# Kernel tuning notes

Hardware: AMD Instinct MI355X
Metric: run time of the kernel (lower is better)

Reference implementation:

```python
import jax, jax.numpy as jnp
import numpy as np

N = 100000          # number of graph nodes
NNZ = 1_600_000     # edges (nnz of sparse adjacency), avg degree 16
D_IN = 512
D_OUT = 128


def setup_inputs() -> dict:
    key = jax.random.key(0)
    kx, kw, kv, kr, kc = jax.random.split(key, 5)
    stdv = 1.0 / np.sqrt(D_IN)  # matches module's init(): uniform(-stdv, stdv)
    x = jax.random.normal(kx, (N, D_IN), dtype=jnp.float32)
    W = jax.random.uniform(kw, (D_IN, D_OUT), minval=-stdv, maxval=stdv, dtype=jnp.float32)
    b = jnp.zeros((D_OUT,), dtype=jnp.float32)
    # Sparse adjacency in COO form: adj[row[e], col[e]] = vals[e]
    vals = jax.random.uniform(kv, (NNZ,), dtype=jnp.float32)
    row = jax.random.randint(kr, (NNZ,), 0, N, dtype=jnp.int64)
    col = jax.random.randint(kc, (NNZ,), 0, N, dtype=jnp.int64)
    return {"x": x, "W": W, "b": b, "vals": vals, "row": row, "col": col}


def reference(x, W, b, vals, row, col):
    # support = self.W(input)  -> dense linear projection [N, D_OUT]
    support = x @ W + b
    # output = torch.spmm(adj, support): out[r] = sum_e adj[r, c_e] * support[c_e]
    msgs = vals[:, None] * support[col]          # [NNZ, D_OUT] gather + scale
    out = jax.ops.segment_sum(msgs, row, num_segments=x.shape[0])  # scatter-add
    return out
```

## Files before the change

kernel.cpp:

```cpp
#include <hip/hip_runtime.h>
#include <hip/hip_bf16.h>

#define D_IN  512
#define D_OUT 128
#define FB_SHIFT 7
#define SB_SHIFT 14
#define NB_S 8
#define MAXFB 800
#define NFH 800
#define CHUNK 4096
#define CAP2 2560
#define MAXE (CAP2 / 256)

typedef __attribute__((ext_vector_type(8))) short bf16x8;
typedef __attribute__((ext_vector_type(4))) float f32x4;
typedef __attribute__((ext_vector_type(8))) short s16x8;

static __device__ inline short f2bs(float f) {
    __hip_bfloat16 h = __float2bfloat16(f);
    return *reinterpret_cast<short*>(&h);
}

__global__ __launch_bounds__(256) void wt_prep(const float* __restrict__ W,
                                               short* __restrict__ Wt,
                                               int* __restrict__ fhist) {
    int idx = blockIdx.x * 256 + threadIdx.x;
    if (idx < D_IN * D_OUT) {
        int k = idx >> 7, c = idx & 127;
        Wt[(long)c * D_IN + k] = f2bs(W[idx]);
    }
    if (blockIdx.x == 0)
        for (int i = threadIdx.x; i < NFH; i += 256) fhist[i] = 0;
}

__global__ __launch_bounds__(256) void fhist_kernel(const int* __restrict__ row,
                                                    int* __restrict__ fhist,
                                                    int nnz, int nfb) {
    __shared__ int lh[NFH];
    const int t = threadIdx.x;
    for (int i = t; i < nfb; i += 256) lh[i] = 0;
    __syncthreads();
    const int base = blockIdx.x * CHUNK;
    const int end = min(base + CHUNK, nnz);
    for (int i = base + t; i < end; i += 256)
        atomicAdd(&lh[row[i] >> FB_SHIFT], 1);
    __syncthreads();
    for (int i = t; i < nfb; i += 256) {
        int c = lh[i];
        if (c) atomicAdd(&fhist[i], c);
    }
}

__global__ __launch_bounds__(256) void fscan(const int* __restrict__ fhist,
                                             int* __restrict__ foffs,
                                             int* __restrict__ scursor,
                                             int* __restrict__ gcursor,
                                             int nfb, int nnz) {
    __shared__ int sdata[256];
    const int t = threadIdx.x;
    int c[4]; int s = 0;
#pragma unroll
    for (int j = 0; j < 4; ++j) {
        int i = t * 4 + j;
        c[j] = (i < nfb) ? fhist[i] : 0;
        s += c[j];
    }
    sdata[t] = s;
    __syncthreads();
    for (int off = 1; off < 256; off <<= 1) {
        int v = (t >= off) ? sdata[t - off] : 0;
        __syncthreads();
        sdata[t] += v;
        __syncthreads();
    }
    int excl = (t == 0) ? 0 : sdata[t - 1];
#pragma unroll
    for (int j = 0; j < 4; ++j) {
        int i = t * 4 + j;
        if (i < nfb) {
            foffs[i] = excl;
            gcursor[i] = excl;
            if ((i & 127) == 0) scursor[i >> 7] = excl;
        }
        excl += c[j];
    }
    if (t == 0) foffs[nfb] = nnz;
}

__global__ __launch_bounds__(256) void sscatter(
    const int* __restrict__ row, const int* __restrict__ col,
    const float* __restrict__ vals, int* __restrict__ scursor,
    int2* __restrict__ evt, int nnz)
{
    __shared__ int hist[NB_S], lbase[NB_S], gbase[NB_S], lcur[NB_S];
    __shared__ int2 stage[CHUNK];
    const int t = threadIdx.x;
    const int base = blockIdx.x * CHUNK;
    const int nloc = min(CHUNK, nnz - base);
    if (t < NB_S) hist[t] = 0;
    __syncthreads();

    int myr[CHUNK / 256];
#pragma unroll
    for (int j = 0; j < CHUNK / 256; ++j) {
        int e = base + t + j * 256;
        myr[j] = (e < nnz) ? row[e] : -1;
        if (myr[j] >= 0) atomicAdd(&hist[myr[j] >> SB_SHIFT], 1);
    }
    __syncthreads();
    if (t == 0) {
        int run = 0;
#pragma unroll
        for (int s = 0; s < NB_S; ++s) {
            lbase[s] = run; lcur[s] = run;
            int c = hist[s];
            gbase[s] = c ? atomicAdd(&scursor[s], c) : 0;
            run += c;
        }
    }
    __syncthreads();
#pragma unroll
    for (int j = 0; j < CHUNK / 256; ++j) {
        int e = base + t + j * 256;
        if (e < nnz) {
            int slot = atomicAdd(&lcur[myr[j] >> SB_SHIFT], 1);
            stage[slot] = make_int2(((myr[j] & 16383) << 17) | col[e],
                                    __float_as_int(vals[e]));
        }
    }
    __syncthreads();
#pragma unroll
    for (int j = 0; j < CHUNK / 256; ++j) {
        int s = t + j * 256;
        if (s < nloc) {
            int sb = 0;
#pragma unroll
            for (int q = 1; q < NB_S; ++q) if (s >= lbase[q]) sb = q;
            evt[gbase[sb] + (s - lbase[sb])] = stage[s];
        }
    }
}

__global__ __launch_bounds__(256) void fscatter(
    const int2* __restrict__ evt, const int* __restrict__ foffs,
    int* __restrict__ gcursor, int2* __restrict__ ev, int nnz, int nfb)
{
    __shared__ int hist[MAXFB], lbase[MAXFB], gbase[MAXFB];
    __shared__ int ssum[256];
    __shared__ int sbpos[NB_S + 1];
    __shared__ int2 stage[CHUNK];
    __shared__ short sbkt[CHUNK];
    const int t = threadIdx.x;
    const int base = blockIdx.x * CHUNK;
    const int nloc = min(CHUNK, nnz - base);

    for (int i = t; i < nfb; i += 256) hist[i] = 0;
    if (t <= NB_S) {
        int fi = t << 7;
        sbpos[t] = foffs[fi > nfb ? nfb : fi];
    }
    __syncthreads();

    int2 mypay[CHUNK / 256];
    int myfb[CHUNK / 256];
#pragma unroll
    for (int j = 0; j < CHUNK / 256; ++j) {
        int p = base + t + j * 256;
        if (p < nnz) {
            mypay[j] = evt[p];
            int sb = 0;
#pragma unroll
            for (int q = 1; q < NB_S; ++q) if (p >= sbpos[q]) sb = q;
            myfb[j] = sb * 128 + ((mypay[j].x >> 17) >> 7);
            atomicAdd(&hist[myfb[j]], 1);
        } else myfb[j] = -1;
    }
    __syncthreads();

    int c[4], s = 0;
#pragma unroll
    for (int j = 0; j < 4; ++j) {
        int i = t * 4 + j;
        c[j] = (i < nfb) ? hist[i] : 0;
        s += c[j];
    }
    ssum[t] = s;
    __syncthreads();
    for (int off = 1; off < 256; off <<= 1) {
        int v = (t >= off) ? ssum[t - off] : 0;
        __syncthreads();
        ssum[t] += v;
        __syncthreads();
    }
    int excl = (t == 0) ? 0 : ssum[t - 1];
#pragma unroll
    for (int j = 0; j < 4; ++j) {
        int i = t * 4 + j;
        if (i < nfb) {
            lbase[i] = excl;
            gbase[i] = c[j] ? atomicAdd(&gcursor[i], c[j]) : 0;
        }
        excl += c[j];
    }
    __syncthreads();
    for (int i = t; i < nfb; i += 256) hist[i] = lbase[i];
    __syncthreads();

#pragma unroll
    for (int j = 0; j < CHUNK / 256; ++j) {
        if (myfb[j] >= 0) {
            int slot = atomicAdd(&hist[myfb[j]], 1);
            stage[slot] = mypay[j];
            sbkt[slot] = (short)myfb[j];
        }
    }
    __syncthreads();
#pragma unroll
    for (int j = 0; j < CHUNK / 256; ++j) {
        int s2 = t + j * 256;
        if (s2 < nloc) {
            int fb = sbkt[s2];
            ev[gbase[fb] + (s2 - lbase[fb])] = stage[s2];
        }
    }
}

__global__ __launch_bounds__(256) void bspmm(
    const int* __restrict__ foffs, const int2* __restrict__ ev,
    const __hip_bfloat16* __restrict__ supb, float* __restrict__ out, int n)
{
    __shared__ int rcnt[128];
    __shared__ int rbase[129];
    __shared__ int lcur[128];
    __shared__ int2 stage[CAP2];
    const int bk = blockIdx.x;
    const int t = threadIdx.x;
    const int r0 = bk << FB_SHIFT;
    const int rend = min(r0 + 128, n);
    const int nrow = rend - r0;
    const int g0 = foffs[bk];
    const int g1 = foffs[bk + 1];
    const int ne = g1 - g0;

    const int w   = t >> 6, l = t & 63;
    const int g   = l >> 4;
    const int sub = l & 15;

    if (ne <= CAP2) {
        if (t < 128) rcnt[t] = 0;
        __syncthreads();
        int2 myq[MAXE]; int myrl[MAXE];
#pragma unroll
        for (int j = 0; j < MAXE; ++j) {
            int i = t + j * 256;
            myrl[j] = -1;
            if (i < ne) {
                myq[j] = ev[g0 + i];
                myrl[j] = (myq[j].x >> 17) & 127;
                atomicAdd(&rcnt[myrl[j]], 1);
            }
        }
        __syncthreads();
        if (t < 128) lcur[t] = rcnt[t];
        __syncthreads();
        for (int off = 1; off < 128; off <<= 1) {
            int u = (t < 128 && t >= off) ? lcur[t - off] : 0;
            __syncthreads();
            if (t < 128) lcur[t] += u;
            __syncthreads();
        }
        if (t < 128) rbase[t + 1] = lcur[t];
        if (t == 0) rbase[0] = 0;
        __syncthreads();
        if (t < 128) lcur[t] = rbase[t];
        __syncthreads();
#pragma unroll
        for (int j = 0; j < MAXE; ++j) {
            if (myrl[j] >= 0) {
                int slot = atomicAdd(&lcur[myrl[j]], 1);
                stage[slot] = myq[j];
            }
        }
        __syncthreads();

        for (int rr = w; rr < nrow; rr += 4) {
            const int r = r0 + rr;
            const int e0 = rbase[rr];
            const int e1 = rbase[rr + 1];
            float acc[8];
#pragma unroll
            for (int i = 0; i < 8; ++i) acc[i] = 0.f;

            auto fma_edge = [&](const int2 q) {
                const s16x8 sv = *reinterpret_cast<const s16x8*>(
                    supb + (long)(q.x & 0x1FFFF) * D_OUT + sub * 8);
                const float v = __int_as_float(q.y);
                const __hip_bfloat162* hp = reinterpret_cast<const __hip_bfloat162*>(&sv);
#pragma unroll
                for (int i = 0; i < 4; ++i) {
                    const float2 f = __bfloat1622float2(hp[i]);
                    acc[2 * i]     += v * f.x;
                    acc[2 * i + 1] += v * f.y;
                }
            };

            int e = e0;
            for (; e + 16 <= e1; e += 16) {
                const int2 q0 = stage[e + g];
                const int2 q1 = stage[e + 4 + g];
                const int2 q2 = stage[e + 8 + g];
                const int2 q3 = stage[e + 12 + g];
                fma_edge(q0); fma_edge(q1); fma_edge(q2); fma_edge(q3);
            }
            for (; e + 4 <= e1; e += 4) {
                fma_edge(stage[e + g]);
            }
            const int rem = e1 - e;
            if (g < rem) fma_edge(stage[e + g]);

#pragma unroll
            for (int i = 0; i < 8; ++i) {
                acc[i] += __shfl_xor(acc[i], 16);
                acc[i] += __shfl_xor(acc[i], 32);
            }
            if (g == 0) {
                float4 o0 = make_float4(acc[0], acc[1], acc[2], acc[3]);
                float4 o1 = make_float4(acc[4], acc[5], acc[6], acc[7]);
                float* op = out + (long)r * D_OUT + sub * 8;
                *reinterpret_cast<float4*>(op) = o0;
                *reinterpret_cast<float4*>(op + 4) = o1;
            }
        }
    } else {
        for (int rr = w; rr < nrow; rr += 4) {
            const int r = r0 + rr;
            const int rl = r & 127;
            float ax = 0.f, ay = 0.f;
            for (int e = g0; e < g1; ++e) {
                const int2 q = ev[e];
                if (((q.x >> 17) & 127) == rl) {
                    const float v = __int_as_float(q.y);
                    const __hip_bfloat162 sh = *reinterpret_cast<const __hip_bfloat162*>(
                        supb + (long)(q.x & 0x1FFFF) * D_OUT + l * 2);
                    const float2 f = __bfloat1622float2(sh);
                    ax += v * f.x;
                    ay += v * f.y;
                }
            }
            *reinterpret_cast<float2*>(out + (long)r * D_OUT + l * 2) =
                make_float2(ax, ay);
        }
    }
}

__global__ __launch_bounds__(256) void gemm_mfma(
    const float* __restrict__ x,
    const short* __restrict__ Wt,
    const float* __restrict__ b,
    __hip_bfloat16* __restrict__ supb,
    int n_nodes)
{
    __shared__ s16x8 A_c[2][4 * 128];
    __shared__ s16x8 B_c[2][4 * 128];

    const int tid  = threadIdx.x;
    const int wave = tid >> 6;
    const int lane = tid & 63;
    const int ln16 = lane & 15;
    const int kb   = lane >> 4;
    const int row0 = blockIdx.x * 128;

    const int srow = tid >> 2;
    const int skc  = tid & 3;

    float4 areg[2][2];
    s16x8  breg[2];

    auto load_A = [&](int k0) {
#pragma unroll
        for (int j = 0; j < 2; ++j) {
            int r = row0 + srow + j * 64;
            r = (r < n_nodes) ? r : (n_nodes - 1);
            const float* p = x + (long)r * D_IN + k0 + skc * 8;
            areg[j][0] = *reinterpret_cast<const float4*>(p);
            areg[j][1] = *reinterpret_cast<const float4*>(p + 4);
        }
    };
    auto load_B = [&](int k0) {
#pragma unroll
        for (int j = 0; j < 2; ++j) {
            int c = srow + j * 64;
            breg[j] = *reinterpret_cast<const s16x8*>(Wt + (long)c * D_IN + k0 + skc * 8);
        }
    };
    auto write_AB = [&](int buf) {
#pragma unroll
        for (int j = 0; j < 2; ++j) {
            const int r = srow + j * 64;
            s16x8 v;
            v[0] = f2bs(areg[j][0].x); v[1] = f2bs(areg[j][0].y);
            v[2] = f2bs(areg[j][0].z); v[3] = f2bs(areg[j][0].w);
            v[4] = f2bs(areg[j][1].x); v[5] = f2bs(areg[j][1].y);
            v[6] = f2bs(areg[j][1].z); v[7] = f2bs(areg[j][1].w);
            A_c[buf][skc * 128 + (r ^ skc)] = v;
            B_c[buf][skc * 128 + (r ^ skc)] = breg[j];
        }
    };

    f32x4 acc[2][8];
#pragma unroll
    for (int rg = 0; rg < 2; ++rg)
#pragma unroll
        for (int t = 0; t < 8; ++t) acc[rg][t] = (f32x4){0.f, 0.f, 0.f, 0.f};

    auto compute = [&](int buf) {
        bf16x8 af[2];
#pragma unroll
        for (int rg = 0; rg < 2; ++rg) {
            const int r = wave * 32 + rg * 16 + ln16;
            const s16x8 v = A_c[buf][kb * 128 + (r ^ kb)];
            af[rg] = *reinterpret_cast<const bf16x8*>(&v);
        }
#pragma unroll
        for (int t = 0; t < 8; ++t) {
            const int c = t * 16 + ln16;
            const s16x8 vb = B_c[buf][kb * 128 + (c ^ kb)];
            const bf16x8 bf = *reinterpret_cast<const bf16x8*>(&vb);
            acc[0][t] = __builtin_amdgcn_mfma_f32_16x16x32_bf16(af[0], bf, acc[0][t], 0, 0, 0);
            acc[1][t] = __builtin_amdgcn_mfma_f32_16x16x32_bf16(af[1], bf, acc[1][t], 0, 0, 0);
        }
    };

    load_A(0);
    load_B(0);
    write_AB(0);
    __syncthreads();

    for (int ks = 0; ks < 15; ++ks) {
        const int cur = ks & 1, nxt = cur ^ 1;
        load_A((ks + 1) * 32);
        load_B((ks + 1) * 32);
        compute(cur);
        write_AB(nxt);
        __syncthreads();
    }
    compute(1);

#pragma unroll
    for (int t = 0; t < 8; ++t) {
        const int col = t * 16 + ln16;
        const float bias = b[col];
#pragma unroll
        for (int rg = 0; rg < 2; ++rg) {
#pragma unroll
            for (int r = 0; r < 4; ++r) {
                const int rr = row0 + wave * 32 + rg * 16 + kb * 4 + r;
                if (rr < n_nodes)
                    supb[(long)rr * D_OUT + col] = __float2bfloat16(acc[rg][t][r] + bias);
            }
        }
    }
}

__global__ __launch_bounds__(256) void spmm_atomic(
    const __hip_bfloat16* __restrict__ supb, const float* __restrict__ vals,
    const int* __restrict__ row, const int* __restrict__ col,
    float* __restrict__ out, int nnz)
{
    long gidx = (long)blockIdx.x * 256 + threadIdx.x;
    int e = (int)(gidx >> 7);
    int d = (int)(gidx & 127);
    if (e < nnz) {
        atomicAdd(&out[(long)row[e] * D_OUT + d],
                  vals[e] * __bfloat162float(supb[(long)col[e] * D_OUT + d]));
    }
}

extern "C" void kernel_launch(void* const* d_in, const int* in_sizes, int n_in,
                              void* d_out, int out_size, void* d_ws, size_t ws_size,
                              hipStream_t stream) {
    const float* x    = (const float*)d_in[0];
    const float* W    = (const float*)d_in[1];
    const float* b    = (const float*)d_in[2];
    const float* vals = (const float*)d_in[3];
    const int*   row  = (const int*)d_in[4];
    const int*   col  = (const int*)d_in[5];
    float* out = (float*)d_out;

    const int n_nodes = in_sizes[0] / D_IN;
    const int nnz     = in_sizes[3];
    const int nfb     = (n_nodes + 127) >> FB_SHIFT;

    auto align_up = [](size_t v) { return (v + 255) & ~(size_t)255; };
    char* wsb = (char*)d_ws;
    size_t off = 0;
    __hip_bfloat16* supb = (__hip_bfloat16*)(wsb + off);
    off = align_up(off + (size_t)n_nodes * D_OUT * 2);
    short* Wt = (short*)(wsb + off);
    off = align_up(off + (size_t)D_OUT * D_IN * 2);
    const size_t need_fallback = off;
    int* fhist   = (int*)(wsb + off); off = align_up(off + (size_t)NFH * 4);
    int* foffs   = (int*)(wsb + off); off = align_up(off + (size_t)(nfb + 1) * 4);
    int* scursor = (int*)(wsb + off); off = align_up(off + NB_S * 4);
    int* gcursor = (int*)(wsb + off); off = align_up(off + (size_t)nfb * 4);
    int2* evt    = (int2*)(wsb + off); off = align_up(off + (size_t)nnz * 8);
    int2* ev     = (int2*)(wsb + off); off = align_up(off + (size_t)nnz * 8);
    const size_t need_full = off;

    if (ws_size >= need_full && nfb <= MAXFB) {
        const int nchunks = (nnz + CHUNK - 1) / CHUNK;
        wt_prep<<<dim3((D_IN * D_OUT) / 256), dim3(256), 0, stream>>>(W, Wt, fhist);
        fhist_kernel<<<dim3(nchunks), dim3(256), 0, stream>>>(row, fhist, nnz, nfb);
        fscan<<<dim3(1), dim3(256), 0, stream>>>(fhist, foffs, scursor, gcursor,
                                                 nfb, nnz);
        gemm_mfma<<<dim3((n_nodes + 127) / 128), dim3(256), 0, stream>>>(
            x, Wt, b, supb, n_nodes);
        sscatter<<<dim3(nchunks), dim3(256), 0, stream>>>(
            row, col, vals, scursor, evt, nnz);
        fscatter<<<dim3(nchunks), dim3(256), 0, stream>>>(
            evt, foffs, gcursor, ev, nnz, nfb);
        bspmm<<<dim3(nfb), dim3(256), 0, stream>>>(foffs, ev, supb, out, n_nodes);
    } else if (ws_size >= need_fallback) {
        wt_prep<<<dim3((D_IN * D_OUT) / 256), dim3(256), 0, stream>>>(W, Wt, fhist);
        gemm_mfma<<<dim3((n_nodes + 127) / 128), dim3(256), 0, stream>>>(
            x, Wt, b, supb, n_nodes);
        hipMemsetAsync(out, 0, (size_t)out_size * 4, stream);
        long total = (long)nnz * D_OUT;
        spmm_atomic<<<dim3((int)((total + 255) / 256)), dim3(256), 0, stream>>>(
            supb, vals, row, col, out, nnz);
    }
}
```

Measured before the change: 222.8 us.

## Fuse edge histogram, scan and two scatter passes into one cooperative kernel

```diff
diff --git a/kernel.cpp b/kernel.cpp
--- a/kernel.cpp
+++ b/kernel.cpp
@@ -1,5 +1,8 @@
 #include <hip/hip_runtime.h>
 #include <hip/hip_bf16.h>
+#include <hip/hip_cooperative_groups.h>
+
+namespace cg = cooperative_groups;
 
 #define D_IN  512
 #define D_OUT 128
@@ -7,7 +10,6 @@
 #define SB_SHIFT 14
 #define NB_S 8
 #define MAXFB 800
-#define NFH 800
 #define CHUNK 4096
 #define CAP2 2560
 #define MAXE (CAP2 / 256)
@@ -22,99 +24,99 @@
 }
 
 __global__ __launch_bounds__(256) void wt_prep(const float* __restrict__ W,
-                                               short* __restrict__ Wt,
-                                               int* __restrict__ fhist) {
+                                               short* __restrict__ Wt) {
     int idx = blockIdx.x * 256 + threadIdx.x;
-    if (idx < D_IN * D_OUT) {
-        int k = idx >> 7, c = idx & 127;
-        Wt[(long)c * D_IN + k] = f2bs(W[idx]);
-    }
-    if (blockIdx.x == 0)
-        for (int i = threadIdx.x; i < NFH; i += 256) fhist[i] = 0;
-}
-
-__global__ __launch_bounds__(256) void fhist_kernel(const int* __restrict__ row,
-                                                    int* __restrict__ fhist,
-                                                    int nnz, int nfb) {
-    __shared__ int lh[NFH];
+    int k = idx >> 7, c = idx & 127;
+    Wt[(long)c * D_IN + k] = f2bs(W[idx]);
+}
+
+__global__ __launch_bounds__(256, 2) void edge_pipe(
+    const int* __restrict__ row, const int* __restrict__ col,
+    const float* __restrict__ vals,
+    int* __restrict__ fhist, int* __restrict__ foffs,
+    int* __restrict__ scursor, int* __restrict__ gcursor,
+    int2* __restrict__ evt, int2* __restrict__ ev,
+    int nnz, int nfb)
+{
+    __shared__ int2 stage[CHUNK];
+    __shared__ short sbkt[CHUNK];
+    __shared__ int hA[MAXFB];
+    __shared__ int hB[MAXFB];
+    __shared__ int hC[MAXFB];
+    __shared__ int ssum[256];
+    __shared__ int sbpos[NB_S + 1];
+    __shared__ int sh[NB_S], slb[NB_S], sgb[NB_S], slc[NB_S];
+
     const int t = threadIdx.x;
-    for (int i = t; i < nfb; i += 256) lh[i] = 0;
-    __syncthreads();
-    const int base = blockIdx.x * CHUNK;
-    const int end = min(base + CHUNK, nnz);
-    for (int i = base + t; i < end; i += 256)
-        atomicAdd(&lh[row[i] >> FB_SHIFT], 1);
-    __syncthreads();
-    for (int i = t; i < nfb; i += 256) {
-        int c = lh[i];
-        if (c) atomicAdd(&fhist[i], c);
-    }
-}
-
-__global__ __launch_bounds__(256) void fscan(const int* __restrict__ fhist,
-                                             int* __restrict__ foffs,
-                                             int* __restrict__ scursor,
-                                             int* __restrict__ gcursor,
-                                             int nfb, int nnz) {
-    __shared__ int sdata[256];
-    const int t = threadIdx.x;
-    int c[4]; int s = 0;
-#pragma unroll
-    for (int j = 0; j < 4; ++j) {
-        int i = t * 4 + j;
-        c[j] = (i < nfb) ? fhist[i] : 0;
-        s += c[j];
-    }
-    sdata[t] = s;
-    __syncthreads();
-    for (int off = 1; off < 256; off <<= 1) {
-        int v = (t >= off) ? sdata[t - off] : 0;
-        __syncthreads();
-        sdata[t] += v;
-        __syncthreads();
-    }
-    int excl = (t == 0) ? 0 : sdata[t - 1];
-#pragma unroll
-    for (int j = 0; j < 4; ++j) {
-        int i = t * 4 + j;
-        if (i < nfb) {
-            foffs[i] = excl;
-            gcursor[i] = excl;
-            if ((i & 127) == 0) scursor[i >> 7] = excl;
-        }
-        excl += c[j];
-    }
-    if (t == 0) foffs[nfb] = nnz;
-}
-
-__global__ __launch_bounds__(256) void sscatter(
-    const int* __restrict__ row, const int* __restrict__ col,
-    const float* __restrict__ vals, int* __restrict__ scursor,
-    int2* __restrict__ evt, int nnz)
-{
-    __shared__ int hist[NB_S], lbase[NB_S], gbase[NB_S], lcur[NB_S];
-    __shared__ int2 stage[CHUNK];
-    const int t = threadIdx.x;
-    const int base = blockIdx.x * CHUNK;
+    const int blk = blockIdx.x;
+    const int base = blk * CHUNK;
     const int nloc = min(CHUNK, nnz - base);
-    if (t < NB_S) hist[t] = 0;
-    __syncthreads();
-
+    cg::grid_group grid = cg::this_grid();
+
+    for (int i = t; i < nfb; i += 256) hA[i] = 0;
+    __syncthreads();
     int myr[CHUNK / 256];
 #pragma unroll
     for (int j = 0; j < CHUNK / 256; ++j) {
         int e = base + t + j * 256;
         myr[j] = (e < nnz) ? row[e] : -1;
-        if (myr[j] >= 0) atomicAdd(&hist[myr[j] >> SB_SHIFT], 1);
-    }
+        if (myr[j] >= 0) atomicAdd(&hA[myr[j] >> FB_SHIFT], 1);
+    }
+    if (blk == 0)
+        for (int i = t; i < nfb; i += 256) fhist[i] = 0;
+    __syncthreads();
+    grid.sync();
+
+    for (int i = t; i < nfb; i += 256) {
+        int c = hA[i];
+        if (c) atomicAdd(&fhist[i], c);
+    }
+    grid.sync();
+
+    if (blk == 0) {
+        int c[4]; int s = 0;
+#pragma unroll
+        for (int j = 0; j < 4; ++j) {
+            int i = t * 4 + j;
+            c[j] = (i < nfb) ? fhist[i] : 0;
+            s += c[j];
+        }
+        ssum[t] = s;
+        __syncthreads();
+        for (int off = 1; off < 256; off <<= 1) {
+            int v = (t >= off) ? ssum[t - off] : 0;
+            __syncthreads();
+            ssum[t] += v;
+            __syncthreads();
+        }
+        int excl = (t == 0) ? 0 : ssum[t - 1];
+#pragma unroll
+        for (int j = 0; j < 4; ++j) {
+            int i = t * 4 + j;
+            if (i < nfb) {
+                foffs[i] = excl;
+                gcursor[i] = excl;
+                if ((i & 127) == 0) scursor[i >> 7] = excl;
+            }
+            excl += c[j];
+        }
+        if (t == 0) foffs[nfb] = nnz;
+    }
+    grid.sync();
+
+    if (t < NB_S) sh[t] = 0;
+    __syncthreads();
+#pragma unroll
+    for (int j = 0; j < CHUNK / 256; ++j)
+        if (myr[j] >= 0) atomicAdd(&sh[myr[j] >> SB_SHIFT], 1);
     __syncthreads();
     if (t == 0) {
         int run = 0;
 #pragma unroll
-        for (int s = 0; s < NB_S; ++s) {
-            lbase[s] = run; lcur[s] = run;
-            int c = hist[s];
-            gbase[s] = c ? atomicAdd(&scursor[s], c) : 0;
+        for (int s2 = 0; s2 < NB_S; ++s2) {
+            slb[s2] = run; slc[s2] = run;
+            int c = sh[s2];
+            sgb[s2] = c ? atomicAdd(&scursor[s2], c) : 0;
             run += c;
         }
     }
@@ -122,8 +124,8 @@
 #pragma unroll
     for (int j = 0; j < CHUNK / 256; ++j) {
         int e = base + t + j * 256;
-        if (e < nnz) {
-            int slot = atomicAdd(&lcur[myr[j] >> SB_SHIFT], 1);
+        if (myr[j] >= 0) {
+            int slot = atomicAdd(&slc[myr[j] >> SB_SHIFT], 1);
             stage[slot] = make_int2(((myr[j] & 16383) << 17) | col[e],
                                     __float_as_int(vals[e]));
         }
@@ -131,36 +133,22 @@
     __syncthreads();
 #pragma unroll
     for (int j = 0; j < CHUNK / 256; ++j) {
-        int s = t + j * 256;
-        if (s < nloc) {
+        int s2 = t + j * 256;
+        if (s2 < nloc) {
             int sb = 0;
 #pragma unroll
-            for (int q = 1; q < NB_S; ++q) if (s >= lbase[q]) sb = q;
-            evt[gbase[sb] + (s - lbase[sb])] = stage[s];
-        }
-    }
-}
-
-__global__ __launch_bounds__(256) void fscatter(
-    const int2* __restrict__ evt, const int* __restrict__ foffs,
-    int* __restrict__ gcursor, int2* __restrict__ ev, int nnz, int nfb)
-{
-    __shared__ int hist[MAXFB], lbase[MAXFB], gbase[MAXFB];
-    __shared__ int ssum[256];
-    __shared__ int sbpos[NB_S + 1];
-    __shared__ int2 stage[CHUNK];
-    __shared__ short sbkt[CHUNK];
-    const int t = threadIdx.x;
-    const int base = blockIdx.x * CHUNK;
-    const int nloc = min(CHUNK, nnz - base);
-
-    for (int i = t; i < nfb; i += 256) hist[i] = 0;
+            for (int q = 1; q < NB_S; ++q) if (s2 >= slb[q]) sb = q;
+            evt[sgb[sb] + (s2 - slb[sb])] = stage[s2];
+        }
+    }
+    grid.sync();
+
+    for (int i = t; i < nfb; i += 256) hA[i] = 0;
     if (t <= NB_S) {
         int fi = t << 7;
         sbpos[t] = foffs[fi > nfb ? nfb : fi];
     }
     __syncthreads();
-
     int2 mypay[CHUNK / 256];
     int myfb[CHUNK / 256];
 #pragma unroll
@@ -172,19 +160,18 @@
 #pragma unroll
             for (int q = 1; q < NB_S; ++q) if (p >= sbpos[q]) sb = q;
             myfb[j] = sb * 128 + ((mypay[j].x >> 17) >> 7);
-            atomicAdd(&hist[myfb[j]], 1);
+            atomicAdd(&hA[myfb[j]], 1);
         } else myfb[j] = -1;
     }
     __syncthreads();
-
-    int c[4], s = 0;
+    int c2[4], s3 = 0;
 #pragma unroll
     for (int j = 0; j < 4; ++j) {
         int i = t * 4 + j;
-        c[j] = (i < nfb) ? hist[i] : 0;
-        s += c[j];
-    }
-    ssum[t] = s;
+        c2[j] = (i < nfb) ? hA[i] : 0;
+        s3 += c2[j];
+    }
+    ssum[t] = s3;
     __syncthreads();
     for (int off = 1; off < 256; off <<= 1) {
         int v = (t >= off) ? ssum[t - off] : 0;
@@ -192,24 +179,23 @@
         ssum[t] += v;
         __syncthreads();
     }
-    int excl = (t == 0) ? 0 : ssum[t - 1];
+    int excl2 = (t == 0) ? 0 : ssum[t - 1];
 #pragma unroll
     for (int j = 0; j < 4; ++j) {
         int i = t * 4 + j;
         if (i < nfb) {
-            lbase[i] = excl;
-            gbase[i] = c[j] ? atomicAdd(&gcursor[i], c[j]) : 0;
-        }
-        excl += c[j];
-    }
-    __syncthreads();
-    for (int i = t; i < nfb; i += 256) hist[i] = lbase[i];
-    __syncthreads();
-
+            hB[i] = excl2;
+            hC[i] = c2[j] ? atomicAdd(&gcursor[i], c2[j]) : 0;
+        }
+        excl2 += c2[j];
+    }
+    __syncthreads();
+    for (int i = t; i < nfb; i += 256) hA[i] = hB[i];
+    __syncthreads();
 #pragma unroll
     for (int j = 0; j < CHUNK / 256; ++j) {
         if (myfb[j] >= 0) {
-            int slot = atomicAdd(&hist[myfb[j]], 1);
+            int slot = atomicAdd(&hA[myfb[j]], 1);
             stage[slot] = mypay[j];
             sbkt[slot] = (short)myfb[j];
         }
@@ -220,7 +206,7 @@
         int s2 = t + j * 256;
         if (s2 < nloc) {
             int fb = sbkt[s2];
-            ev[gbase[fb] + (s2 - lbase[fb])] = stage[s2];
+            ev[hC[fb] + (s2 - hB[fb])] = stage[s2];
         }
     }
 }
@@ -340,9 +326,9 @@
                 const int2 q = ev[e];
                 if (((q.x >> 17) & 127) == rl) {
                     const float v = __int_as_float(q.y);
-                    const __hip_bfloat162 sh = *reinterpret_cast<const __hip_bfloat162*>(
+                    const __hip_bfloat162 sh2 = *reinterpret_cast<const __hip_bfloat162*>(
                         supb + (long)(q.x & 0x1FFFF) * D_OUT + l * 2);
-                    const float2 f = __bfloat1622float2(sh);
+                    const float2 f = __bfloat1622float2(sh2);
                     ax += v * f.x;
                     ay += v * f.y;
                 }
@@ -488,8 +474,8 @@
     float* out = (float*)d_out;
 
     const int n_nodes = in_sizes[0] / D_IN;
-    const int nnz     = in_sizes[3];
-    const int nfb     = (n_nodes + 127) >> FB_SHIFT;
+    int nnz           = in_sizes[3];
+    int nfb           = (n_nodes + 127) >> FB_SHIFT;
 
     auto align_up = [](size_t v) { return (v + 255) & ~(size_t)255; };
     char* wsb = (char*)d_ws;
@@ -499,7 +485,7 @@
     short* Wt = (short*)(wsb + off);
     off = align_up(off + (size_t)D_OUT * D_IN * 2);
     const size_t need_fallback = off;
-    int* fhist   = (int*)(wsb + off); off = align_up(off + (size_t)NFH * 4);
+    int* fhist   = (int*)(wsb + off); off = align_up(off + (size_t)MAXFB * 4);
     int* foffs   = (int*)(wsb + off); off = align_up(off + (size_t)(nfb + 1) * 4);
     int* scursor = (int*)(wsb + off); off = align_up(off + NB_S * 4);
     int* gcursor = (int*)(wsb + off); off = align_up(off + (size_t)nfb * 4);
@@ -509,19 +495,18 @@
 
     if (ws_size >= need_full && nfb <= MAXFB) {
         const int nchunks = (nnz + CHUNK - 1) / CHUNK;
-        wt_prep<<<dim3((D_IN * D_OUT) / 256), dim3(256), 0, stream>>>(W, Wt, fhist);
-        fhist_kernel<<<dim3(nchunks), dim3(256), 0, stream>>>(row, fhist, nnz, nfb);
-        fscan<<<dim3(1), dim3(256), 0, stream>>>(fhist, foffs, scursor, gcursor,
-                                                 nfb, nnz);
+        wt_prep<<<dim3((D_IN * D_OUT) / 256), dim3(256), 0, stream>>>(W, Wt);
         gemm_mfma<<<dim3((n_nodes + 127) / 128), dim3(256), 0, stream>>>(
             x, Wt, b, supb, n_nodes);
-        sscatter<<<dim3(nchunks), dim3(256), 0, stream>>>(
-            row, col, vals, scursor, evt, nnz);
-        fscatter<<<dim3(nchunks), dim3(256), 0, stream>>>(
-            evt, foffs, gcursor, ev, nnz, nfb);
+        void* args[] = {(void*)&row, (void*)&col, (void*)&vals,
+                        (void*)&fhist, (void*)&foffs, (void*)&scursor,
+                        (void*)&gcursor, (void*)&evt, (void*)&ev,
+                        (void*)&nnz, (void*)&nfb};
+        hipLaunchCooperativeKernel((void*)edge_pipe, dim3(nchunks), dim3(256),
+                                   args, 0, stream);
         bspmm<<<dim3(nfb), dim3(256), 0, stream>>>(foffs, ev, supb, out, n_nodes);
     } else if (ws_size >= need_fallback) {
-        wt_prep<<<dim3((D_IN * D_OUT) / 256), dim3(256), 0, stream>>>(W, Wt, fhist);
+        wt_prep<<<dim3((D_IN * D_OUT) / 256), dim3(256), 0, stream>>>(W, Wt);
         gemm_mfma<<<dim3((n_nodes + 127) / 128), dim3(256), 0, stream>>>(
             x, Wt, b, supb, n_nodes);
         hipMemsetAsync(out, 0, (size_t)out_size * 4, stream);
```

Measured after the change: 387.2 us. 1.74x slower.

## Merge weight prep with histogram and fold scan into GEMM launch

Applied to the files above, without the earlier changes.

```diff
diff --git a/kernel.cpp b/kernel.cpp
--- a/kernel.cpp
+++ b/kernel.cpp
@@ -21,70 +21,190 @@
     return *reinterpret_cast<short*>(&h);
 }
 
-__global__ __launch_bounds__(256) void wt_prep(const float* __restrict__ W,
-                                               short* __restrict__ Wt,
-                                               int* __restrict__ fhist) {
-    int idx = blockIdx.x * 256 + threadIdx.x;
-    if (idx < D_IN * D_OUT) {
+__global__ __launch_bounds__(256) void prep_hist(
+    const float* __restrict__ W, short* __restrict__ Wt,
+    const int* __restrict__ row, int* __restrict__ bhist,
+    int nnz, int nfb, int nwt)
+{
+    __shared__ int lh[NFH];
+    const int t = threadIdx.x;
+    if ((int)blockIdx.x < nwt) {
+        int idx = blockIdx.x * 256 + t;
         int k = idx >> 7, c = idx & 127;
         Wt[(long)c * D_IN + k] = f2bs(W[idx]);
-    }
-    if (blockIdx.x == 0)
-        for (int i = threadIdx.x; i < NFH; i += 256) fhist[i] = 0;
-}
-
-__global__ __launch_bounds__(256) void fhist_kernel(const int* __restrict__ row,
-                                                    int* __restrict__ fhist,
-                                                    int nnz, int nfb) {
-    __shared__ int lh[NFH];
-    const int t = threadIdx.x;
+        return;
+    }
+    const int cb = blockIdx.x - nwt;
     for (int i = t; i < nfb; i += 256) lh[i] = 0;
     __syncthreads();
-    const int base = blockIdx.x * CHUNK;
+    const int base = cb * CHUNK;
     const int end = min(base + CHUNK, nnz);
     for (int i = base + t; i < end; i += 256)
         atomicAdd(&lh[row[i] >> FB_SHIFT], 1);
     __syncthreads();
-    for (int i = t; i < nfb; i += 256) {
-        int c = lh[i];
-        if (c) atomicAdd(&fhist[i], c);
-    }
-}
-
-__global__ __launch_bounds__(256) void fscan(const int* __restrict__ fhist,
-                                             int* __restrict__ foffs,
-                                             int* __restrict__ scursor,
-                                             int* __restrict__ gcursor,
-                                             int nfb, int nnz) {
-    __shared__ int sdata[256];
-    const int t = threadIdx.x;
-    int c[4]; int s = 0;
-#pragma unroll
-    for (int j = 0; j < 4; ++j) {
-        int i = t * 4 + j;
-        c[j] = (i < nfb) ? fhist[i] : 0;
-        s += c[j];
-    }
-    sdata[t] = s;
-    __syncthreads();
-    for (int off = 1; off < 256; off <<= 1) {
-        int v = (t >= off) ? sdata[t - off] : 0;
-        __syncthreads();
-        sdata[t] += v;
-        __syncthreads();
-    }
-    int excl = (t == 0) ? 0 : sdata[t - 1];
-#pragma unroll
-    for (int j = 0; j < 4; ++j) {
-        int i = t * 4 + j;
-        if (i < nfb) {
-            foffs[i] = excl;
-            gcursor[i] = excl;
-            if ((i & 127) == 0) scursor[i >> 7] = excl;
-        }
-        excl += c[j];
-    }
-    if (t == 0) foffs[nfb] = nnz;
+    for (int i = t; i < nfb; i += 256)
+        bhist[(size_t)cb * NFH + i] = lh[i];
+}
+
+__global__ __launch_bounds__(256) void gemm_fscan(
+    const float* __restrict__ x,
+    const short* __restrict__ Wt,
+    const float* __restrict__ b,
+    __hip_bfloat16* __restrict__ supb,
+    int n_nodes,
+    const int* __restrict__ bhist,
+    int* __restrict__ foffs,
+    int* __restrict__ scursor,
+    int* __restrict__ gcursor,
+    int nfb, int nnz, int nchunks, int ngemm)
+{
+    __shared__ s16x8 A_c[2][4 * 128];
+    __shared__ s16x8 B_c[2][4 * 128];
+
+    const int tid  = threadIdx.x;
+
+    if ((int)blockIdx.x >= ngemm) {
+        int* sdata = reinterpret_cast<int*>(A_c);
+        const int t = tid;
+        int c[4];
+        if (t * 4 + 3 < nfb) {
+            int4 a4 = make_int4(0, 0, 0, 0);
+            for (int cb = 0; cb < nchunks; ++cb) {
+                const int4 v = *reinterpret_cast<const int4*>(
+                    bhist + (size_t)cb * NFH + t * 4);
+                a4.x += v.x; a4.y += v.y; a4.z += v.z; a4.w += v.w;
+            }
+            c[0] = a4.x; c[1] = a4.y; c[2] = a4.z; c[3] = a4.w;
+        } else {
+#pragma unroll
+            for (int j = 0; j < 4; ++j) {
+                int i = t * 4 + j; int s = 0;
+                if (i < nfb)
+                    for (int cb = 0; cb < nchunks; ++cb)
+                        s += bhist[(size_t)cb * NFH + i];
+                c[j] = s;
+            }
+        }
+        int s = c[0] + c[1] + c[2] + c[3];
+        sdata[t] = s;
+        __syncthreads();
+        for (int off = 1; off < 256; off <<= 1) {
+            int v = (t >= off) ? sdata[t - off] : 0;
+            __syncthreads();
+            sdata[t] += v;
+            __syncthreads();
+        }
+        int excl = (t == 0) ? 0 : sdata[t - 1];
+#pragma unroll
+        for (int j = 0; j < 4; ++j) {
+            int i = t * 4 + j;
+            if (i < nfb) {
+                foffs[i] = excl;
+                gcursor[i] = excl;
+                if ((i & 127) == 0) scursor[i >> 7] = excl;
+            }
+            excl += c[j];
+        }
+        if (t == 0) foffs[nfb] = nnz;
+        return;
+    }
+
+    const int wave = tid >> 6;
+    const int lane = tid & 63;
+    const int ln16 = lane & 15;
+    const int kb   = lane >> 4;
+    const int row0 = blockIdx.x * 128;
+
+    const int srow = tid >> 2;
+    const int skc  = tid & 3;
+
+    float4 areg[2][2];
+    s16x8  breg[2];
+
+    auto load_A = [&](int k0) {
+#pragma unroll
+        for (int j = 0; j < 2; ++j) {
+            int r = row0 + srow + j * 64;
+            r = (r < n_nodes) ? r : (n_nodes - 1);
+            const float* p = x + (long)r * D_IN + k0 + skc * 8;
+            areg[j][0] = *reinterpret_cast<const float4*>(p);
+            areg[j][1] = *reinterpret_cast<const float4*>(p + 4);
+        }
+    };
+    auto load_B = [&](int k0) {
+#pragma unroll
+        for (int j = 0; j < 2; ++j) {
+            int c = srow + j * 64;
+            breg[j] = *reinterpret_cast<const s16x8*>(Wt + (long)c * D_IN + k0 + skc * 8);
+        }
+    };
+    auto write_AB = [&](int buf) {
+#pragma unroll
+        for (int j = 0; j < 2; ++j) {
+            const int r = srow + j * 64;
+            s16x8 v;
+            v[0] = f2bs(areg[j][0].x); v[1] = f2bs(areg[j][0].y);
+            v[2] = f2bs(areg[j][0].z); v[3] = f2bs(areg[j][0].w);
+            v[4] = f2bs(areg[j][1].x); v[5] = f2bs(areg[j][1].y);
+            v[6] = f2bs(areg[j][1].z); v[7] = f2bs(areg[j][1].w);
+            A_c[buf][skc * 128 + (r ^ skc)] = v;
+            B_c[buf][skc * 128 + (r ^ skc)] = breg[j];
+        }
+    };
+
+    f32x4 acc[2][8];
+#pragma unroll
+    for (int rg = 0; rg < 2; ++rg)
+#pragma unroll
+        for (int t = 0; t < 8; ++t) acc[rg][t] = (f32x4){0.f, 0.f, 0.f, 0.f};
+
+    auto compute = [&](int buf) {
+        bf16x8 af[2];
+#pragma unroll
+        for (int rg = 0; rg < 2; ++rg) {
+            const int r = wave * 32 + rg * 16 + ln16;
+            const s16x8 v = A_c[buf][kb * 128 + (r ^ kb)];
+            af[rg] = *reinterpret_cast<const bf16x8*>(&v);
+        }
+#pragma unroll
+        for (int t = 0; t < 8; ++t) {
+            const int c = t * 16 + ln16;
+            const s16x8 vb = B_c[buf][kb * 128 + (c ^ kb)];
+            const bf16x8 bf = *reinterpret_cast<const bf16x8*>(&vb);
+            acc[0][t] = __builtin_amdgcn_mfma_f32_16x16x32_bf16(af[0], bf, acc[0][t], 0, 0, 0);
+            acc[1][t] = __builtin_amdgcn_mfma_f32_16x16x32_bf16(af[1], bf, acc[1][t], 0, 0, 0);
+        }
+    };
+
+    load_A(0);
+    load_B(0);
+    write_AB(0);
+    __syncthreads();
+
+    for (int ks = 0; ks < 15; ++ks) {
+        const int cur = ks & 1, nxt = cur ^ 1;
+        load_A((ks + 1) * 32);
+        load_B((ks + 1) * 32);
+        compute(cur);
+        write_AB(nxt);
+        __syncthreads();
+    }
+    compute(1);
+
+#pragma unroll
+    for (int t = 0; t < 8; ++t) {
+        const int col = t * 16 + ln16;
+        const float bias = b[col];
+#pragma unroll
+        for (int rg = 0; rg < 2; ++rg) {
+#pragma unroll
+            for (int r = 0; r < 4; ++r) {
+                const int rr = row0 + wave * 32 + rg * 16 + kb * 4 + r;
+                if (rr < n_nodes)
+                    supb[(long)rr * D_OUT + col] = __float2bfloat16(acc[rg][t][r] + bias);
+            }
+        }
+    }
 }
 
 __global__ __launch_bounds__(256) void sscatter(
@@ -353,115 +473,6 @@
     }
 }
 
-__global__ __launch_bounds__(256) void gemm_mfma(
-    const float* __restrict__ x,
-    const short* __restrict__ Wt,
-    const float* __restrict__ b,
-    __hip_bfloat16* __restrict__ supb,
-    int n_nodes)
-{
-    __shared__ s16x8 A_c[2][4 * 128];
-    __shared__ s16x8 B_c[2][4 * 128];
-
-    const int tid  = threadIdx.x;
-    const int wave = tid >> 6;
-    const int lane = tid & 63;
-    const int ln16 = lane & 15;
-    const int kb   = lane >> 4;
-    const int row0 = blockIdx.x * 128;
-
-    const int srow = tid >> 2;
-    const int skc  = tid & 3;
-
-    float4 areg[2][2];
-    s16x8  breg[2];
-
-    auto load_A = [&](int k0) {
-#pragma unroll
-        for (int j = 0; j < 2; ++j) {
-            int r = row0 + srow + j * 64;
-            r = (r < n_nodes) ? r : (n_nodes - 1);
-            const float* p = x + (long)r * D_IN + k0 + skc * 8;
-            areg[j][0] = *reinterpret_cast<const float4*>(p);
-            areg[j][1] = *reinterpret_cast<const float4*>(p + 4);
-        }
-    };
-    auto load_B = [&](int k0) {
-#pragma unroll
-        for (int j = 0; j < 2; ++j) {
-            int c = srow + j * 64;
-            breg[j] = *reinterpret_cast<const s16x8*>(Wt + (long)c * D_IN + k0 + skc * 8);
-        }
-    };
-    auto write_AB = [&](int buf) {
-#pragma unroll
-        for (int j = 0; j < 2; ++j) {
-            const int r = srow + j * 64;
-            s16x8 v;
-            v[0] = f2bs(areg[j][0].x); v[1] = f2bs(areg[j][0].y);
-            v[2] = f2bs(areg[j][0].z); v[3] = f2bs(areg[j][0].w);
-            v[4] = f2bs(areg[j][1].x); v[5] = f2bs(areg[j][1].y);
-            v[6] = f2bs(areg[j][1].z); v[7] = f2bs(areg[j][1].w);
-            A_c[buf][skc * 128 + (r ^ skc)] = v;
-            B_c[buf][skc * 128 + (r ^ skc)] = breg[j];
-        }
-    };
-
-    f32x4 acc[2][8];
-#pragma unroll
-    for (int rg = 0; rg < 2; ++rg)
-#pragma unroll
-        for (int t = 0; t < 8; ++t) acc[rg][t] = (f32x4){0.f, 0.f, 0.f, 0.f};
-
-    auto compute = [&](int buf) {
-        bf16x8 af[2];
-#pragma unroll
-        for (int rg = 0; rg < 2; ++rg) {
-            const int r = wave * 32 + rg * 16 + ln16;
-            const s16x8 v = A_c[buf][kb * 128 + (r ^ kb)];
-            af[rg] = *reinterpret_cast<const bf16x8*>(&v);
-        }
-#pragma unroll
-        for (int t = 0; t < 8; ++t) {
-            const int c = t * 16 + ln16;
-            const s16x8 vb = B_c[buf][kb * 128 + (c ^ kb)];
-            const bf16x8 bf = *reinterpret_cast<const bf16x8*>(&vb);
-            acc[0][t] = __builtin_amdgcn_mfma_f32_16x16x32_bf16(af[0], bf, acc[0][t], 0, 0, 0);
-            acc[1][t] = __builtin_amdgcn_mfma_f32_16x16x32_bf16(af[1], bf, acc[1][t], 0, 0, 0);
-        }
-    };
-
-    load_A(0);
-    load_B(0);
-    write_AB(0);
-    __syncthreads();
-
-    for (int ks = 0; ks < 15; ++ks) {
-        const int cur = ks & 1, nxt = cur ^ 1;
-        load_A((ks + 1) * 32);
-        load_B((ks + 1) * 32);
-        compute(cur);
-        write_AB(nxt);
-        __syncthreads();
-    }
-    compute(1);
-
-#pragma unroll
-    for (int t = 0; t < 8; ++t) {
-        const int col = t * 16 + ln16;
-        const float bias = b[col];
-#pragma unroll
-        for (int rg = 0; rg < 2; ++rg) {
-#pragma unroll
-            for (int r = 0; r < 4; ++r) {
-                const int rr = row0 + wave * 32 + rg * 16 + kb * 4 + r;
-                if (rr < n_nodes)
-                    supb[(long)rr * D_OUT + col] = __float2bfloat16(acc[rg][t][r] + bias);
-            }
-        }
-    }
-}
-
 __global__ __launch_bounds__(256) void spmm_atomic(
     const __hip_bfloat16* __restrict__ supb, const float* __restrict__ vals,
     const int* __restrict__ row, const int* __restrict__ col,
@@ -490,6 +501,9 @@
     const int n_nodes = in_sizes[0] / D_IN;
     const int nnz     = in_sizes[3];
     const int nfb     = (n_nodes + 127) >> FB_SHIFT;
+    const int nch     = (nnz + CHUNK - 1) / CHUNK;
+    const int nwt     = (D_IN * D_OUT) / 256;
+    const int ngemm   = (n_nodes + 127) / 128;
 
     auto align_up = [](size_t v) { return (v + 255) & ~(size_t)255; };
     char* wsb = (char*)d_ws;
@@ -499,7 +513,7 @@
     short* Wt = (short*)(wsb + off);
     off = align_up(off + (size_t)D_OUT * D_IN * 2);
     const size_t need_fallback = off;
-    int* fhist   = (int*)(wsb + off); off = align_up(off + (size_t)NFH * 4);
+    int* bhist   = (int*)(wsb + off); off = align_up(off + (size_t)nch * NFH * 4);
     int* foffs   = (int*)(wsb + off); off = align_up(off + (size_t)(nfb + 1) * 4);
     int* scursor = (int*)(wsb + off); off = align_up(off + NB_S * 4);
     int* gcursor = (int*)(wsb + off); off = align_up(off + (size_t)nfb * 4);
@@ -508,22 +522,22 @@
     const size_t need_full = off;
 
     if (ws_size >= need_full && nfb <= MAXFB) {
-        const int nchunks = (nnz + CHUNK - 1) / CHUNK;
-        wt_prep<<<dim3((D_IN * D_OUT) / 256), dim3(256), 0, stream>>>(W, Wt, fhist);
-        fhist_kernel<<<dim3(nchunks), dim3(256), 0, stream>>>(row, fhist, nnz, nfb);
-        fscan<<<dim3(1), dim3(256), 0, stream>>>(fhist, foffs, scursor, gcursor,
-                                                 nfb, nnz);
-        gemm_mfma<<<dim3((n_nodes + 127) / 128), dim3(256), 0, stream>>>(
-            x, Wt, b, supb, n_nodes);
-        sscatter<<<dim3(nchunks), dim3(256), 0, stream>>>(
+        prep_hist<<<dim3(nwt + nch), dim3(256), 0, stream>>>(
+            W, Wt, row, bhist, nnz, nfb, nwt);
+        gemm_fscan<<<dim3(ngemm + 1), dim3(256), 0, stream>>>(
+            x, Wt, b, supb, n_nodes, bhist, foffs, scursor, gcursor,
+            nfb, nnz, nch, ngemm);
+        sscatter<<<dim3(nch), dim3(256), 0, stream>>>(
             row, col, vals, scursor, evt, nnz);
-        fscatter<<<dim3(nchunks), dim3(256), 0, stream>>>(
+        fscatter<<<dim3(nch), dim3(256), 0, stream>>>(
             evt, foffs, gcursor, ev, nnz, nfb);
         bspmm<<<dim3(nfb), dim3(256), 0, stream>>>(foffs, ev, supb, out, n_nodes);
     } else if (ws_size >= need_fallback) {
-        wt_prep<<<dim3((D_IN * D_OUT) / 256), dim3(256), 0, stream>>>(W, Wt, fhist);
-        gemm_mfma<<<dim3((n_nodes + 127) / 128), dim3(256), 0, stream>>>(
-            x, Wt, b, supb, n_nodes);
+        prep_hist<<<dim3(nwt), dim3(256), 0, stream>>>(
+            W, Wt, row, (int*)d_ws, 0, nfb, nwt);
+        gemm_fscan<<<dim3(ngemm), dim3(256), 0, stream>>>(
+            x, Wt, b, supb, n_nodes, (int*)d_ws, (int*)d_ws, (int*)d_ws,
+            (int*)d_ws, nfb, nnz, 0, ngemm);
         hipMemsetAsync(out, 0, (size_t)out_size * 4, stream);
         long total = (long)nnz * D_OUT;
         spmm_atomic<<<dim3((int)((total + 255) / 256)), dim3(256), 0, stream>>>(
```

Measured after the change: 309.8 us. 1.39x slower.
